# Performance work log

Measured on AMD Instinct MI355X. Metric: run time of the kernel, lower is better.

The kernel has to match this reference:

```python
import jax, jax.numpy as jnp
import numpy as np

ISIZE = 512; NHEAD = 8; NNOD = 8; MAXP = 5; NEDGE = 34; TAU = 1.0; EPS = 1e-6
B = 4; SLEN = 1024

def _ln(x, g, b):
    m = x.mean(-1, keepdims=True)
    v = ((x - m) ** 2).mean(-1, keepdims=True)
    return (x - m) * jax.lax.rsqrt(v + EPS) * g + b

def _qmask(nsrc):
    # q_mask_full: edge 0 (encoder source) is masked out for the q path
    m = np.zeros((nsrc, 5), bool); m[0, :] = True
    return m.reshape(-1)

def _routing(node_p, edge_p):
    # Host-side argmax routing; mirrors the .item() syncs in the torch forward.
    node_p = np.asarray(node_p); edge_p = np.asarray(edge_p)
    routes, lind = [], 0
    for c in range(NNOD):
        nsrc = min(c + 2, MAXP); snode = c - nsrc
        ep = edge_p[:, lind:lind + nsrc, :].reshape(3, -1)
        qm = _qmask(nsrc)
        nact = int(np.argmax(node_p[c]))
        qsel = int(np.argmax(np.where(qm, -np.inf, ep[0])))
        r = dict(lind=lind, nsrc=nsrc, snode=snode, act=nact, q=qsel, k=None, v=None, ktype=None, km=None, vmode=None)
        if nact < 7:
            km = qm if nact > 0 else None
            kl = ep[1] if km is None else np.where(km, -np.inf, ep[1])
            r['k'] = int(np.argmax(kl)); r['km'] = km
            r['ktype'] = -2 if r['k'] // 5 == 0 else -1
            if nact < 5:
                if nact == 0 and r['ktype'] == -2:
                    r['v'] = int(np.argmax(ep[2][:5])); r['vmode'] = 'first5'
                else:
                    vl = ep[2] if km is None else np.where(km, -np.inf, ep[2])
                    r['v'] = int(np.argmax(vl)); r['vmode'] = 'full'
        routes.append(r); lind += nsrc
    return routes

def _selw(logits, mask, sel):
    # GumbleNormDrop (eval): softmax over masked logits, weight of selected entry
    if mask is not None:
        logits = jnp.where(jnp.asarray(mask), -jnp.inf, logits)
    return jax.nn.softmax(logits / TAU)[sel]

def _edge_op(x, e, op, eW, eb, eg, ebe):
    # ops 0/1/2: LN->Linear with relu/gelu/identity (cost isize^2+3*isize); 3: Linear; 4: identity
    if op == 4:
        return x
    if op == 3:
        return x @ eW[e] + eb[e]
    h = _ln(x, eg[e], ebe[e]) @ eW[e] + eb[e]
    return jax.nn.relu(h) if op == 0 else (jax.nn.gelu(h) if op == 1 else h)

def _mha(q, k, v, Wn, bn, gn, bln, mask):
    Bq, Sq, D = q.shape; dh = D // NHEAD; Sk = k.shape[1]
    qn = _ln(q, gn, bln)
    qh = (qn @ Wn[0] + bn[0]).reshape(Bq, Sq, NHEAD, dh).transpose(0, 2, 1, 3)
    kh = (k @ Wn[1] + bn[1]).reshape(Bq, Sk, NHEAD, dh).transpose(0, 2, 1, 3)
    vh = (v @ Wn[2] + bn[2]).reshape(Bq, v.shape[1], NHEAD, dh).transpose(0, 2, 1, 3)
    s = jnp.einsum('bhqd,bhkd->bhqk', qh, kh) / np.float32(np.sqrt(dh))
    if mask is not None:
        s = jnp.where(mask[:, :, None, :], -1e9, s)  # [B,1,Sk] -> [B,1,1,Sk]
    o = jnp.einsum('bhqk,bhkd->bhqd', jax.nn.softmax(s, -1), vh)
    o = o.transpose(0, 2, 1, 3).reshape(Bq, Sq, D)
    return q + o @ Wn[3] + bn[3]

def _node_op(q, k, v, act, Wn, bn, gn, bln, mask):
    if act == 0: return _mha(q, k, v, Wn, bn, gn, bln, mask)
    if act == 1: return q + (jax.nn.gelu(q @ Wn[0] + bn[0]) * (k @ Wn[1] + bn[1])) @ Wn[3] + bn[3]
    if act == 2: return _ln(q + k + v, gn, bln)
    if act == 3: return q + jax.nn.relu(q @ Wn[0] + k @ Wn[1] + v @ Wn[2]) @ Wn[3] + bn[3]
    if act == 4: return q * jax.nn.sigmoid(k) + v
    if act == 5: return q + jax.nn.gelu(k @ Wn[1] + bn[1])
    if act == 6: return q + k
    return _ln(q, gn, bln)  # act 7: unary

def _forward(inpute, inputo, node_p, edge_p, eW, eb, eg, ebe, nW, nb, ng, nbe, og, obe, src_pad_mask, tgt_pad_mask, routes):
    outs = {-2: inpute, -1: inputo}
    processed = set()
    for c, r in enumerate(routes):
        lind, snode = r['lind'], r['snode']
        epq, epk, epv = (edge_p[i, lind:lind + r['nsrc'], :].reshape(-1) for i in range(3))
        qm = _qmask(r['nsrc'])
        aw = jax.nn.softmax(node_p[c] / TAU)[r['act']]
        def take(sel, logits, mask):
            se, op = sel // 5, sel % 5
            inn = -2 if se == 0 else snode + se
            processed.add(inn)
            return _selw(logits, mask, sel) * _edge_op(outs[inn], lind + se, op, eW, eb, eg, ebe)
        qv = take(r['q'], epq, qm)
        kv = take(r['k'], epk, r['km']) if r['k'] is not None else None
        if r['v'] is None:
            vv = None
        elif r['vmode'] == 'first5':
            vv = take(r['v'], epv[:5], None)
        else:
            vv = take(r['v'], epv, r['km'])
        mask = None if r['act'] == 7 else (tgt_pad_mask if r['ktype'] == -1 else src_pad_mask)
        outs[c] = aw * _node_op(qv, kv, vv, r['act'], nW[c], nb[c], ng[c], nbe[c], mask)
    rem = [outs[i] for i in range(NNOD) if i not in processed]
    o = rem[0]
    for t in rem[1:]:
        o = o + t
    return _ln(o, og, obe)

def setup_inputs():
    key = jax.random.key(0)
    ks = jax.random.split(key, 8)
    s = 0.02
    return {
        'inpute': jax.random.normal(ks[0], (B, SLEN, ISIZE), jnp.float32),
        'inputo': jax.random.normal(ks[1], (B, SLEN, ISIZE), jnp.float32),
        'node_p': jax.random.normal(ks[2], (NNOD, 8), jnp.float32),
        'edge_p': jax.random.normal(ks[3], (3, NEDGE, 5), jnp.float32),
        'edge_W': jax.random.normal(ks[4], (NEDGE, ISIZE, ISIZE), jnp.float32) * s,
        'edge_b': jnp.zeros((NEDGE, ISIZE), jnp.float32),
        'edge_g': jnp.ones((NEDGE, ISIZE), jnp.float32),
        'edge_beta': jnp.zeros((NEDGE, ISIZE), jnp.float32),
        'node_W': jax.random.normal(ks[5], (NNOD, 4, ISIZE, ISIZE), jnp.float32) * s,
        'node_b': jnp.zeros((NNOD, 4, ISIZE), jnp.float32),
        'node_g': jnp.ones((NNOD, ISIZE), jnp.float32),
        'node_beta': jnp.zeros((NNOD, ISIZE), jnp.float32),
        'out_g': jnp.ones((ISIZE,), jnp.float32),
        'out_beta': jnp.zeros((ISIZE,), jnp.float32),
        'src_pad_mask': jnp.zeros((B, 1, SLEN), bool),
        'tgt_pad_mask': jnp.zeros((B, 1, SLEN), bool),
    }

def reference(inpute, inputo, node_p, edge_p, edge_W, edge_b, edge_g, edge_beta, node_W, node_b, node_g, node_beta, out_g, out_beta, src_pad_mask, tgt_pad_mask):
    routes = _routing(node_p, edge_p)
    return _forward(inpute, inputo, node_p, edge_p, edge_W, edge_b, edge_g, edge_beta, node_W, node_b, node_g, node_beta, out_g, out_beta, src_pad_mask, tgt_pad_mask, routes)
```

## Files before the change

kernel.cpp:

```cpp
#include <hip/hip_runtime.h>
#include <hip/hip_bf16.h>
#include <math.h>

#define NTOK 4096
#define DIM  512
#define NNODC 8
#define NEDGEC 34

typedef unsigned short u16;
typedef unsigned int   u32;

typedef __attribute__((ext_vector_type(8))) short bf16x8;
typedef __attribute__((ext_vector_type(4))) float f32x4;

__device__ __forceinline__ float b2f(u16 u){ return __uint_as_float(((u32)u) << 16); }
__device__ __forceinline__ u16 f2b(float f){
    u32 x = __float_as_uint(f);
    u32 r = x + 0x7FFFu + ((x >> 16) & 1u);
    return (u16)(r >> 16);
}
__device__ __forceinline__ float ldp(const void* p, int i, int isbf){
    return isbf ? b2f(((const u16*)p)[i]) : ((const float*)p)[i];
}
__device__ __forceinline__ float gelu_t(float x){
    float x3 = x*x*x;
    return 0.5f*x*(1.0f + tanhf(0.7978845608028654f*(x + 0.044715f*x3)));
}
__device__ __forceinline__ float sigm(float x){ return 1.0f/(1.0f + expf(-x)); }

typedef __attribute__((address_space(3))) void lds_vp;
typedef __attribute__((address_space(1))) const void gbl_vp;
__device__ __forceinline__ void gload16(const u16* g, u16* l){
    __builtin_amdgcn_global_load_lds((gbl_vp*)g, (lds_vp*)l, 16, 0, 0);
}

struct Routes {
    int isbf;
    int act[NNODC];
    int q_slot[NNODC], q_e[NNODC], q_op[NNODC];
    int k_has[NNODC], k_slot[NNODC], k_e[NNODC], k_op[NNODC];
    int v_has[NNODC], v_slot[NNODC], v_e[NNODC], v_op[NNODC];
    float aw[NNODC], qw[NNODC], kw[NNODC], vw[NNODC];
    int used[NNODC];
};

__global__ void routing_kernel(const void* __restrict__ node_p,
                               const void* __restrict__ edge_p,
                               const u32* __restrict__ edge_g_probe,
                               Routes* R){
    __shared__ float ep[3*NEDGEC*5 + 2];
    __shared__ float np[NNODC*8];
    __shared__ int used_s[NNODC];
    const int tid = threadIdx.x;
    const int isbf = (edge_g_probe[0] == 0x3F803F80u) ? 1 : 0;
    for (int i = tid; i < 3*NEDGEC*5; i += 64) ep[i] = ldp(edge_p, i, isbf);
    if (tid < NNODC*8) np[tid] = ldp(node_p, tid, isbf);
    if (tid < NNODC) used_s[tid] = 0;
    __syncthreads();

    if (tid < NNODC){
        const int c = tid;
        int lind = 0;
        for (int i = 0; i < c; i++) lind += (i + 2 < 5) ? (i + 2) : 5;
        const int nsrc  = (c + 2 < 5) ? (c + 2) : 5;
        const int snode = c - nsrc;
        const int n     = nsrc * 5;

        float bm = -INFINITY; int nact = 0;
        for (int j = 0; j < 8; j++){
            float v = np[c*8 + j];
            if (v > bm){ bm = v; nact = j; }
        }
        float ssum = 0.f;
        for (int j = 0; j < 8; j++) ssum += __expf(np[c*8 + j] - bm);
        R->act[c] = nact;
        R->aw[c]  = __expf(np[c*8 + nact] - bm) / ssum;

        auto sel = [&](int phase, int nn, int maskFirst5, int* selOut, float* wOut){
            float best = -INFINITY; int bi = 0;
            for (int s2 = 0; s2 < nn; s2++){
                if (maskFirst5 && s2 < 5) continue;
                float v = ep[phase*NEDGEC*5 + (lind + s2/5)*5 + (s2%5)];
                if (v > best){ best = v; bi = s2; }
            }
            float ss = 0.f;
            for (int s2 = 0; s2 < nn; s2++){
                if (maskFirst5 && s2 < 5) continue;
                ss += __expf(ep[phase*NEDGEC*5 + (lind + s2/5)*5 + (s2%5)] - best);
            }
            *selOut = bi; *wOut = 1.0f / ss;
        };

        int qsel; float qw_;
        sel(0, n, 1, &qsel, &qw_);
        int se = qsel / 5;
        int inn = (se == 0) ? -2 : (snode + se);
        R->q_op[c] = qsel % 5; R->q_e[c] = lind + se; R->q_slot[c] = inn + 2;
        R->qw[c] = qw_;
        if (inn >= 0) used_s[inn] = 1;
        if (nact < 7){
            const int mk = (nact > 0) ? 1 : 0;
            int ksel; float kw_;
            sel(1, n, mk, &ksel, &kw_);
            se = ksel / 5; inn = (se == 0) ? -2 : (snode + se);
            R->k_has[c] = 1; R->k_op[c] = ksel % 5; R->k_e[c] = lind + se;
            R->k_slot[c] = inn + 2; R->kw[c] = kw_;
            if (inn >= 0) used_s[inn] = 1;
            if (nact < 5){
                int vsel; float vw_;
                if (nact == 0 && ksel < 5) sel(2, 5, 0, &vsel, &vw_);
                else                        sel(2, n, mk, &vsel, &vw_);
                se = vsel / 5; inn = (se == 0) ? -2 : (snode + se);
                R->v_has[c] = 1; R->v_op[c] = vsel % 5; R->v_e[c] = lind + se;
                R->v_slot[c] = inn + 2; R->vw[c] = vw_;
                if (inn >= 0) used_s[inn] = 1;
            } else { R->v_has[c] = 0; R->vw[c] = 0.f; }
        } else { R->k_has[c] = 0; R->v_has[c] = 0; R->kw[c] = 0.f; R->vw[c] = 0.f; }
    }
    __syncthreads();
    if (tid < NNODC) R->used[tid] = used_s[tid];
    if (tid == 0) R->isbf = isbf;
}

__global__ __launch_bounds__(256) void transpose_w(const void* __restrict__ eW,
                                                   const void* __restrict__ nW,
                                                   const u32* __restrict__ probe,
                                                   u16* __restrict__ Wt){
    __shared__ float tile[32][33];
    const int isbf = (probe[0] == 0x3F803F80u) ? 1 : 0;
    const int mat = blockIdx.z;
    const void* src = (mat < NEDGEC) ? eW : nW;
    const size_t moff = (size_t)((mat < NEDGEC) ? mat : (mat - NEDGEC)) * DIM * DIM;
    const int k0 = blockIdx.x*32, n0 = blockIdx.y*32;
    const int tx = threadIdx.x & 31, ty = threadIdx.x >> 5;
    #pragma unroll
    for (int r = 0; r < 32; r += 8){
        const size_t off = moff + (size_t)(k0 + r + ty)*DIM + n0 + tx;
        tile[r + ty][tx] = isbf ? b2f(((const u16*)src)[off]) : ((const float*)src)[off];
    }
    __syncthreads();
    #pragma unroll
    for (int r = 0; r < 32; r += 8){
        const size_t off = (size_t)mat*DIM*DIM + (size_t)(n0 + r + ty)*DIM + k0 + tx;
        Wt[off] = f2b(tile[tx][r + ty]);
    }
}

__global__ __launch_bounds__(256) void convert_in(const Routes* __restrict__ R,
                                                  const void* __restrict__ ie,
                                                  const void* __restrict__ io,
                                                  u16* __restrict__ Xb0,
                                                  u16* __restrict__ Xb1){
    const size_t base = ((size_t)blockIdx.x*256 + threadIdx.x) * 8;
    if (R->isbf){
        *(uint4*)(Xb0 + base) = *(const uint4*)((const u16*)ie + base);
        *(uint4*)(Xb1 + base) = *(const uint4*)((const u16*)io + base);
    } else {
        const float* a = (const float*)ie + base;
        const float* b = (const float*)io + base;
        u16 oa[8], ob[8];
        #pragma unroll
        for (int j = 0; j < 8; j++){ oa[j] = f2b(a[j]); ob[j] = f2b(b[j]); }
        *(uint4*)(Xb0 + base) = *(const uint4*)oa;
        *(uint4*)(Xb1 + base) = *(const uint4*)ob;
    }
}

struct __align__(16) LGS { u16 A[2][64*64]; u16 B[2][64*64]; };

__device__ void lean_gemm(LGS& sm, int isbf, int nsrc, int m0, int n0,
        const u16* __restrict__ A0, const u16* __restrict__ A1, const u16* __restrict__ A2,
        const u16* __restrict__ W0, const u16* __restrict__ W1, const u16* __restrict__ W2,
        const void* bias, int actMode,
        const u16* __restrict__ residB, float scale,
        u16* __restrict__ outB)
{
    const int tid = threadIdx.x;
    const int w = tid >> 6, lane = tid & 63;
    const int wr = w >> 1, wc = w & 1;
    const int l15 = lane & 15, quad = lane >> 4;
    const int NT = nsrc * 8;

    const int rsw = lane >> 3;
    const int c16 = lane & 7;
    const int rA  = w*16 + rsw;
    const size_t kcol = (size_t)((c16 ^ rsw) << 3);

    auto stage = [&](int buf, int it){
        const int s = it >> 3, kt = it & 7;
        const u16* Ab = (s == 0) ? A0 : ((s == 1) ? A1 : A2);
        const u16* Wb = (s == 0) ? W0 : ((s == 1) ? W1 : W2);
        const size_t ka = (size_t)kt*64 + kcol;
        const u16* ga = Ab + (size_t)(m0 + rA)*DIM + ka;
        const u16* gb = Wb + (size_t)(n0 + rA)*DIM + ka;
        u16* la = &sm.A[buf][rA*64 + c16*8];
        u16* lb = &sm.B[buf][rA*64 + c16*8];
        gload16(ga,          la);
        gload16(ga + 8*DIM,  la + 8*64);
        gload16(gb,          lb);
        gload16(gb + 8*DIM,  lb + 8*64);
    };

    f32x4 acc[2][2];
    #pragma unroll
    for (int i = 0; i < 2; i++)
        #pragma unroll
        for (int j = 0; j < 2; j++) acc[i][j] = (f32x4){0.f,0.f,0.f,0.f};

    stage(0, 0);
    __syncthreads();

    for (int it = 0; it < NT; it++){
        const int buf = it & 1;
        if (it + 1 < NT) stage(buf ^ 1, it + 1);
        #pragma unroll
        for (int kc = 0; kc < 2; kc++){
            const int sl = (((kc*4 + quad) ^ (l15 & 7)) << 3);
            bf16x8 af0 = *(const bf16x8*)&sm.A[buf][(wr*32      + l15)*64 + sl];
            bf16x8 af1 = *(const bf16x8*)&sm.A[buf][(wr*32 + 16 + l15)*64 + sl];
            bf16x8 bf0 = *(const bf16x8*)&sm.B[buf][(wc*32      + l15)*64 + sl];
            bf16x8 bf1 = *(const bf16x8*)&sm.B[buf][(wc*32 + 16 + l15)*64 + sl];
            acc[0][0] = __builtin_amdgcn_mfma_f32_16x16x32_bf16(af0, bf0, acc[0][0], 0, 0, 0);
            acc[0][1] = __builtin_amdgcn_mfma_f32_16x16x32_bf16(af0, bf1, acc[0][1], 0, 0, 0);
            acc[1][0] = __builtin_amdgcn_mfma_f32_16x16x32_bf16(af1, bf0, acc[1][0], 0, 0, 0);
            acc[1][1] = __builtin_amdgcn_mfma_f32_16x16x32_bf16(af1, bf1, acc[1][1], 0, 0, 0);
        }
        __syncthreads();
    }

    float* st = (float*)&sm;
    #pragma unroll
    for (int i = 0; i < 2; i++){
        #pragma unroll
        for (int j = 0; j < 2; j++){
            const int rowl = wr*32 + i*16 + quad*4;
            const int coll = wc*32 + j*16 + l15;
            const float bv = bias ? ldp(bias, n0 + coll, isbf) : 0.f;
            #pragma unroll
            for (int rg = 0; rg < 4; rg++){
                float v = acc[i][j][rg] + bv;
                if (actMode == 1) v = fmaxf(v, 0.f);
                else if (actMode == 2) v = gelu_t(v);
                st[(rowl + rg)*68 + coll] = v;
            }
        }
    }
    __syncthreads();
    #pragma unroll
    for (int t = 0; t < 2; t++){
        const int cid = tid + 256*t;
        const int rowl = cid >> 3, cg = (cid & 7)*8;
        float v[8];
        *(float4*)&v[0] = *(const float4*)&st[rowl*68 + cg];
        *(float4*)&v[4] = *(const float4*)&st[rowl*68 + cg + 4];
        const size_t go = (size_t)(m0 + rowl)*DIM + n0 + cg;
        if (residB){
            uint4 ru = *(const uint4*)(residB + go);
            const u16* rp = (const u16*)&ru;
            #pragma unroll
            for (int j2 = 0; j2 < 8; j2++) v[j2] += b2f(rp[j2]);
        }
        u16 o[8];
        #pragma unroll
        for (int j2 = 0; j2 < 8; j2++) o[j2] = f2b(v[j2]*scale);
        *(uint4*)(outB + go) = *(const uint4*)o;
    }
}

__device__ __forceinline__ void tile_remap(int* m0, int* n0){
    const int lin = blockIdx.y*64 + blockIdx.x;
    const int xcd = lin & 7, idx = lin >> 3;
    *m0 = (xcd*8 + (idx & 7)) * 64;
    *n0 = (idx >> 3) * 64;
}

__device__ __forceinline__ const void* subp(const void* p, size_t elemOff, int isbf){
    return isbf ? (const void*)((const u16*)p + elemOff) : (const void*)((const float*)p + elemOff);
}

__global__ __launch_bounds__(256) void edge_prep(const Routes* __restrict__ R, int c,
        const u16* __restrict__ Xb, u16* __restrict__ P,
        const void* eg, const void* ebeta){
    const int z = blockIdx.z;
    int has, op, e, slot;
    if (z == 0){ has = 1;            op = R->q_op[c]; e = R->q_e[c]; slot = R->q_slot[c]; }
    else if (z == 1){ has = R->k_has[c]; op = R->k_op[c]; e = R->k_e[c]; slot = R->k_slot[c]; }
    else        { has = R->v_has[c]; op = R->v_op[c]; e = R->v_e[c]; slot = R->v_slot[c]; }
    if (!has || op >= 3) return;
    const int isbf = R->isbf;
    const int tid = threadIdx.x, wid = tid >> 6, lane = tid & 63;
    const int row = blockIdx.x*4 + wid;
    const u16* src = Xb + (size_t)slot*NTOK*DIM + (size_t)row*DIM;
    u16* dst = P + (size_t)z*NTOK*DIM + (size_t)row*DIM;
    float x[8];
    #pragma unroll
    for (int j = 0; j < 2; j++){
        ushort4 u = *(const ushort4*)(src + lane*4 + j*256);
        x[j*4+0] = b2f(u.x); x[j*4+1] = b2f(u.y); x[j*4+2] = b2f(u.z); x[j*4+3] = b2f(u.w);
    }
    float s = 0.f, q = 0.f;
    #pragma unroll
    for (int j = 0; j < 8; j++){ s += x[j]; q += x[j]*x[j]; }
    #pragma unroll
    for (int m = 1; m < 64; m <<= 1){ s += __shfl_xor(s, m); q += __shfl_xor(q, m); }
    const float mu = s*(1.0f/512.0f);
    const float rstd = rsqrtf(q*(1.0f/512.0f) - mu*mu + 1e-6f);
    #pragma unroll
    for (int j = 0; j < 2; j++){
        const int col = lane*4 + j*256;
        u16 o[4];
        #pragma unroll
        for (int t = 0; t < 4; t++)
            o[t] = f2b((x[j*4+t] - mu)*rstd*ldp(eg, e*DIM + col + t, isbf) + ldp(ebeta, e*DIM + col + t, isbf));
        *(ushort4*)(dst + col) = *(const ushort4*)o;
    }
}

__global__ __launch_bounds__(256, 4) void edge_gemm(const Routes* __restrict__ R, int c,
        const u16* __restrict__ Xb, const u16* __restrict__ P,
        u16* QVb, u16* KVb, u16* VVb,
        const u16* __restrict__ Wt, const void* eb){
    __shared__ LGS sm;
    const int isbf = R->isbf;
    const int z = blockIdx.z;
    int has, slot, e, op; float w; u16* outB;
    if (z == 0){ has = 1;            slot = R->q_slot[c]; e = R->q_e[c]; op = R->q_op[c]; w = R->qw[c]; outB = QVb; }
    else if (z == 1){ has = R->k_has[c]; slot = R->k_slot[c]; e = R->k_e[c]; op = R->k_op[c]; w = R->kw[c]; outB = KVb; }
    else        { has = R->v_has[c]; slot = R->v_slot[c]; e = R->v_e[c]; op = R->v_op[c]; w = R->vw[c]; outB = VVb; }
    if (!has) return;
    if (op == 4){
        const int tid = threadIdx.x;
        const int r = blockIdx.x*64 + (tid >> 2);
        const int c0 = blockIdx.y*64 + (tid & 3)*16;
        const u16* src = Xb + (size_t)slot*NTOK*DIM + (size_t)r*DIM + c0;
        const size_t off = (size_t)r*DIM + c0;
        #pragma unroll
        for (int t = 0; t < 2; t++){
            uint4 u = *(const uint4*)(src + t*8);
            const u16* up = (const u16*)&u;
            u16 o[8];
            #pragma unroll
            for (int j = 0; j < 8; j++) o[j] = f2b(w*b2f(up[j]));
            *(uint4*)(outB + off + t*8) = *(const uint4*)o;
        }
        return;
    }
    const u16* A = (op < 3) ? (P + (size_t)z*NTOK*DIM) : (Xb + (size_t)slot*NTOK*DIM);
    const int actMode = (op == 0) ? 1 : ((op == 1) ? 2 : 0);
    int m0, n0; tile_remap(&m0, &n0);
    lean_gemm(sm, isbf, 1, m0, n0, A, nullptr, nullptr,
              Wt + (size_t)e*DIM*DIM, nullptr, nullptr,
              subp(eb, (size_t)e*DIM, isbf), actMode,
              nullptr, w, outB);
}

__global__ __launch_bounds__(256) void mid1(const Routes* __restrict__ R, int c,
        const u16* __restrict__ QVb, const u16* __restrict__ KVb, const u16* __restrict__ VVb,
        u16* __restrict__ P1, u16* __restrict__ outcb,
        const void* ng, const void* nbeta){
    const int act = R->act[c];
    if (act == 1 || act == 3 || act == 5) return;
    const int isbf = R->isbf;
    const float aw = R->aw[c];
    const int tid = threadIdx.x, wid = tid >> 6, lane = tid & 63;
    const int row = blockIdx.x*4 + wid;
    const size_t roff = (size_t)row*DIM;
    float x[8];
    #pragma unroll
    for (int j = 0; j < 2; j++){
        ushort4 u = *(const ushort4*)(QVb + roff + lane*4 + j*256);
        x[j*4+0] = b2f(u.x); x[j*4+1] = b2f(u.y); x[j*4+2] = b2f(u.z); x[j*4+3] = b2f(u.w);
    }
    if (act == 4 || act == 6 || act == 2){
        float k[8], v[8];
        #pragma unroll
        for (int j = 0; j < 2; j++){
            ushort4 u = *(const ushort4*)(KVb + roff + lane*4 + j*256);
            k[j*4+0] = b2f(u.x); k[j*4+1] = b2f(u.y); k[j*4+2] = b2f(u.z); k[j*4+3] = b2f(u.w);
        }
        if (act != 6){
            #pragma unroll
            for (int j = 0; j < 2; j++){
                ushort4 u = *(const ushort4*)(VVb + roff + lane*4 + j*256);
                v[j*4+0] = b2f(u.x); v[j*4+1] = b2f(u.y); v[j*4+2] = b2f(u.z); v[j*4+3] = b2f(u.w);
            }
        }
        if (act == 4){
            #pragma unroll
            for (int j = 0; j < 2; j++){
                u16 o[4];
                #pragma unroll
                for (int t = 0; t < 4; t++) o[t] = f2b(aw*(x[j*4+t]*sigm(k[j*4+t]) + v[j*4+t]));
                *(ushort4*)(outcb + roff + lane*4 + j*256) = *(const ushort4*)o;
            }
            return;
        }
        if (act == 6){
            #pragma unroll
            for (int j = 0; j < 2; j++){
                u16 o[4];
                #pragma unroll
                for (int t = 0; t < 4; t++) o[t] = f2b(aw*(x[j*4+t] + k[j*4+t]));
                *(ushort4*)(outcb + roff + lane*4 + j*256) = *(const ushort4*)o;
            }
            return;
        }
        #pragma unroll
        for (int j = 0; j < 8; j++) x[j] += k[j] + v[j];
    }
    float s = 0.f, q2 = 0.f;
    #pragma unroll
    for (int j = 0; j < 8; j++){ s += x[j]; q2 += x[j]*x[j]; }
    #pragma unroll
    for (int m = 1; m < 64; m <<= 1){ s += __shfl_xor(s, m); q2 += __shfl_xor(q2, m); }
    const float mu = s*(1.0f/512.0f);
    const float rstd = rsqrtf(q2*(1.0f/512.0f) - mu*mu + 1e-6f);
    const float sc = (act == 0) ? 1.0f : aw;
    u16* dst = (act == 0) ? P1 : outcb;
    #pragma unroll
    for (int j = 0; j < 2; j++){
        const int col = lane*4 + j*256;
        u16 o[4];
        #pragma unroll
        for (int t = 0; t < 4; t++)
            o[t] = f2b(sc*((x[j*4+t] - mu)*rstd*ldp(ng, c*DIM + col + t, isbf) + ldp(nbeta, c*DIM + col + t, isbf)));
        *(ushort4*)(dst + roff + col) = *(const ushort4*)o;
    }
}

__global__ __launch_bounds__(256, 4) void node_gemm_a(const Routes* __restrict__ R, int c,
        const u16* __restrict__ P1, const u16* __restrict__ QVb,
        const u16* __restrict__ KVb, const u16* __restrict__ VVb,
        u16* T1b, u16* T2b, u16* T3b,
        const u16* __restrict__ Wt, const void* nb){
    __shared__ LGS sm;
    const int isbf = R->isbf;
    const int act = R->act[c];
    const int z = blockIdx.z;
    const size_t msz = (size_t)DIM*DIM;
    const u16* W0 = Wt + (NEDGEC + (size_t)c*4 + 0)*msz;
    const u16* W1 = Wt + (NEDGEC + (size_t)c*4 + 1)*msz;
    const u16* W2 = Wt + (NEDGEC + (size_t)c*4 + 2)*msz;
    const void* b0 = subp(nb, (size_t)(c*4 + 0)*DIM, isbf);
    const void* b1 = subp(nb, (size_t)(c*4 + 1)*DIM, isbf);
    const void* b2 = subp(nb, (size_t)(c*4 + 2)*DIM, isbf);
    int m0, n0; tile_remap(&m0, &n0);
    if (z == 0){
        if (act == 0)
            lean_gemm(sm, isbf, 1, m0, n0, P1,0,0, W0,0,0, b0, 0, nullptr, 1.f, T1b);
        else if (act == 1)
            lean_gemm(sm, isbf, 1, m0, n0, QVb,0,0, W0,0,0, b0, 2, nullptr, 1.f, T1b);
        else if (act == 3)
            lean_gemm(sm, isbf, 3, m0, n0, QVb,KVb,VVb, W0,W1,W2, nullptr, 1, nullptr, 1.f, T1b);
    } else if (z == 1){
        if (act == 0 || act == 1)
            lean_gemm(sm, isbf, 1, m0, n0, KVb,0,0, W1,0,0, b1, 0, nullptr, 1.f, T2b);
        else if (act == 5)
            lean_gemm(sm, isbf, 1, m0, n0, KVb,0,0, W1,0,0, b1, 2, nullptr, 1.f, T2b);
    } else {
        if (act == 0)
            lean_gemm(sm, isbf, 1, m0, n0, VVb,0,0, W2,0,0, b2, 0, nullptr, 1.f, T3b);
    }
}

struct __align__(16) FS {
    float Qs[64][68];
    float KPs[64][68];
    float Vs[64][68];
    float red[64*16];
    float mrun[64], lrun[64], alph[64];
};

__global__ __launch_bounds__(256) void mid2(const Routes* __restrict__ R, int c,
        const u16* __restrict__ Q, const u16* __restrict__ K,
        const u16* __restrict__ V, u16* __restrict__ T4b, u16* __restrict__ P4b){
    const int act = R->act[c];
    if (act == 1){
        const int bid = blockIdx.y*32 + blockIdx.x;
        const size_t base = ((size_t)bid*256 + threadIdx.x)*16;
        #pragma unroll
        for (int h = 0; h < 2; h++){
            uint4 ua = *(const uint4*)(Q + base + h*8);
            uint4 ub = *(const uint4*)(K + base + h*8);
            const u16* pa = (const u16*)&ua;
            const u16* pb = (const u16*)&ub;
            u16 o[8];
            #pragma unroll
            for (int j = 0; j < 8; j++) o[j] = f2b(b2f(pa[j]) * b2f(pb[j]));
            *(uint4*)(P4b + base + h*8) = *(const uint4*)o;
        }
        return;
    }
    if (act != 0) return;
    __shared__ FS sm;
    const int tid = threadIdx.x;
    const int tx = tid & 15, ty = tid >> 4;
    const int b = blockIdx.x >> 3, h = blockIdx.x & 7;
    const int q0 = blockIdx.y * 64;
    const size_t baseQ = ((size_t)b*1024 + q0)*DIM + h*64;
    {
        const int r = tid >> 2, ch = tid & 3;
        const u16* qp = Q + baseQ + (size_t)r*DIM + ch*16;
        #pragma unroll
        for (int t = 0; t < 4; t++){
            ushort4 u = *(const ushort4*)(qp + t*4);
            sm.Qs[r][ch*16 + t*4 + 0] = b2f(u.x);
            sm.Qs[r][ch*16 + t*4 + 1] = b2f(u.y);
            sm.Qs[r][ch*16 + t*4 + 2] = b2f(u.z);
            sm.Qs[r][ch*16 + t*4 + 3] = b2f(u.w);
        }
    }
    if (tid < 64){ sm.mrun[tid] = -INFINITY; sm.lrun[tid] = 0.f; }
    float o[4][4];
    #pragma unroll
    for (int i = 0; i < 4; i++)
        #pragma unroll
        for (int j = 0; j < 4; j++) o[i][j] = 0.f;
    __syncthreads();

    for (int kt = 0; kt < 16; kt++){
        const size_t baseK = ((size_t)b*1024 + kt*64)*DIM + h*64;
        {
            const int r = tid >> 2, ch = tid & 3;
            const u16* kp = K + baseK + (size_t)r*DIM + ch*16;
            const u16* vp = V + baseK + (size_t)r*DIM + ch*16;
            #pragma unroll
            for (int t = 0; t < 4; t++){
                ushort4 uk = *(const ushort4*)(kp + t*4);
                ushort4 uv = *(const ushort4*)(vp + t*4);
                sm.KPs[r][ch*16 + t*4 + 0] = b2f(uk.x);
                sm.KPs[r][ch*16 + t*4 + 1] = b2f(uk.y);
                sm.KPs[r][ch*16 + t*4 + 2] = b2f(uk.z);
                sm.KPs[r][ch*16 + t*4 + 3] = b2f(uk.w);
                sm.Vs [r][ch*16 + t*4 + 0] = b2f(uv.x);
                sm.Vs [r][ch*16 + t*4 + 1] = b2f(uv.y);
                sm.Vs [r][ch*16 + t*4 + 2] = b2f(uv.z);
                sm.Vs [r][ch*16 + t*4 + 3] = b2f(uv.w);
            }
        }
        __syncthreads();
        float s[4][4];
        #pragma unroll
        for (int i = 0; i < 4; i++)
            #pragma unroll
            for (int j = 0; j < 4; j++) s[i][j] = 0.f;
        for (int d = 0; d < 64; d += 4){
            float4 qv[4], kv[4];
            #pragma unroll
            for (int i = 0; i < 4; i++) qv[i] = *(const float4*)&sm.Qs[ty*4+i][d];
            #pragma unroll
            for (int j = 0; j < 4; j++) kv[j] = *(const float4*)&sm.KPs[tx*4+j][d];
            #pragma unroll
            for (int i = 0; i < 4; i++)
                #pragma unroll
                for (int j = 0; j < 4; j++)
                    s[i][j] += qv[i].x*kv[j].x + qv[i].y*kv[j].y + qv[i].z*kv[j].z + qv[i].w*kv[j].w;
        }
        #pragma unroll
        for (int i = 0; i < 4; i++)
            #pragma unroll
            for (int j = 0; j < 4; j++) s[i][j] *= 0.125f;
        #pragma unroll
        for (int i = 0; i < 4; i++){
            float mx = fmaxf(fmaxf(s[i][0], s[i][1]), fmaxf(s[i][2], s[i][3]));
            sm.red[(ty*4+i)*16 + tx] = mx;
        }
        __syncthreads();
        if (tid < 64){
            float mt = -INFINITY;
            for (int t = 0; t < 16; t++) mt = fmaxf(mt, sm.red[tid*16+t]);
            float mold = sm.mrun[tid];
            float mnew = fmaxf(mold, mt);
            sm.alph[tid] = expf(mold - mnew);
            sm.mrun[tid] = mnew;
        }
        __syncthreads();
        #pragma unroll
        for (int i = 0; i < 4; i++){
            const float mn = sm.mrun[ty*4+i];
            float ps = 0.f;
            #pragma unroll
            for (int j = 0; j < 4; j++){
                float p = expf(s[i][j] - mn);
                sm.KPs[ty*4+i][tx*4+j] = p;
                ps += p;
            }
            sm.red[(ty*4+i)*16 + tx] = ps;
        }
        __syncthreads();
        if (tid < 64){
            float ss = 0.f;
            for (int t = 0; t < 16; t++) ss += sm.red[tid*16+t];
            sm.lrun[tid] = sm.lrun[tid]*sm.alph[tid] + ss;
        }
        __syncthreads();
        #pragma unroll
        for (int i = 0; i < 4; i++){
            const float a = sm.alph[ty*4+i];
            #pragma unroll
            for (int j = 0; j < 4; j++) o[i][j] *= a;
        }
        for (int k = 0; k < 64; k++){
            float4 v4 = *(const float4*)&sm.Vs[k][tx*4];
            float p0 = sm.KPs[ty*4+0][k];
            float p1 = sm.KPs[ty*4+1][k];
            float p2 = sm.KPs[ty*4+2][k];
            float p3 = sm.KPs[ty*4+3][k];
            o[0][0] += p0*v4.x; o[0][1] += p0*v4.y; o[0][2] += p0*v4.z; o[0][3] += p0*v4.w;
            o[1][0] += p1*v4.x; o[1][1] += p1*v4.y; o[1][2] += p1*v4.z; o[1][3] += p1*v4.w;
            o[2][0] += p2*v4.x; o[2][1] += p2*v4.y; o[2][2] += p2*v4.z; o[2][3] += p2*v4.w;
            o[3][0] += p3*v4.x; o[3][1] += p3*v4.y; o[3][2] += p3*v4.z; o[3][3] += p3*v4.w;
        }
        __syncthreads();
    }
    #pragma unroll
    for (int i = 0; i < 4; i++){
        const float inv = 1.0f / sm.lrun[ty*4+i];
        u16 ov[4];
        #pragma unroll
        for (int j = 0; j < 4; j++) ov[j] = f2b(o[i][j]*inv);
        *(ushort4*)(T4b + baseQ + (size_t)(ty*4+i)*DIM + tx*4) = *(const ushort4*)ov;
    }
}

__global__ __launch_bounds__(256, 4) void node_gemm_b(const Routes* __restrict__ R, int c,
        const u16* __restrict__ QVb, const u16* __restrict__ T1b, const u16* __restrict__ P4b,
        const u16* __restrict__ T4b, const u16* __restrict__ T2b,
        u16* outcb, const u16* __restrict__ Wt, const void* nb){
    const int act = R->act[c];
    const float aw = R->aw[c];
    if (act == 5){
        const int tid = threadIdx.x;
        const int r = blockIdx.x*64 + (tid >> 2);
        const int c0 = blockIdx.y*64 + (tid & 3)*16;
        const size_t off = (size_t)r*DIM + c0;
        #pragma unroll
        for (int t = 0; t < 2; t++){
            uint4 uq = *(const uint4*)(QVb + off + t*8);
            uint4 ug = *(const uint4*)(T2b + off + t*8);
            const u16* pq = (const u16*)&uq;
            const u16* pg = (const u16*)&ug;
            u16 o[8];
            #pragma unroll
            for (int j = 0; j < 8; j++) o[j] = f2b(aw*(b2f(pq[j]) + b2f(pg[j])));
            *(uint4*)(outcb + off + t*8) = *(const uint4*)o;
        }
        return;
    }
    if (!(act == 0 || act == 1 || act == 3)) return;
    __shared__ LGS sm;
    const int isbf = R->isbf;
    const u16* W3 = Wt + (NEDGEC + (size_t)c*4 + 3)*(size_t)DIM*DIM;
    const void* b3 = subp(nb, (size_t)(c*4 + 3)*DIM, isbf);
    const u16* A = (act == 0) ? T4b : ((act == 1) ? P4b : T1b);
    int m0, n0; tile_remap(&m0, &n0);
    lean_gemm(sm, isbf, 1, m0, n0, A, nullptr, nullptr, W3, nullptr, nullptr,
              b3, 0, QVb, aw, outcb);
}

__global__ __launch_bounds__(128) void final_ln(const Routes* __restrict__ R,
        const u16* __restrict__ Xb, const void* og, const void* obeta,
        void* __restrict__ out){
    const int isbf = R->isbf;
    const int row = blockIdx.x, tid = threadIdx.x;
    const size_t off = (size_t)row*DIM + tid*4;
    float x0 = 0.f, x1 = 0.f, x2 = 0.f, x3 = 0.f;
    for (int cc = 0; cc < NNODC; cc++){
        if (R->used[cc]) continue;
        ushort4 u = *(const ushort4*)(Xb + (size_t)(2 + cc)*NTOK*DIM + off);
        x0 += b2f(u.x); x1 += b2f(u.y); x2 += b2f(u.z); x3 += b2f(u.w);
    }
    __shared__ float rs_[128], rq_[128];
    rs_[tid] = x0 + x1 + x2 + x3;
    rq_[tid] = x0*x0 + x1*x1 + x2*x2 + x3*x3;
    __syncthreads();
    for (int st = 64; st > 0; st >>= 1){
        if (tid < st){ rs_[tid] += rs_[tid+st]; rq_[tid] += rq_[tid+st]; }
        __syncthreads();
    }
    float m = rs_[0]*(1.0f/512.0f);
    float var = rq_[0]*(1.0f/512.0f) - m*m;
    float rstd = rsqrtf(var + 1e-6f);
    float o0 = (x0 - m)*rstd*ldp(og, tid*4+0, isbf) + ldp(obeta, tid*4+0, isbf);
    float o1 = (x1 - m)*rstd*ldp(og, tid*4+1, isbf) + ldp(obeta, tid*4+1, isbf);
    float o2 = (x2 - m)*rstd*ldp(og, tid*4+2, isbf) + ldp(obeta, tid*4+2, isbf);
    float o3 = (x3 - m)*rstd*ldp(og, tid*4+3, isbf) + ldp(obeta, tid*4+3, isbf);
    if (isbf){
        u16 o[4] = { f2b(o0), f2b(o1), f2b(o2), f2b(o3) };
        *(ushort4*)((u16*)out + off) = *(const ushort4*)o;
    } else {
        float4 o; o.x = o0; o.y = o1; o.z = o2; o.w = o3;
        *(float4*)((float*)out + off) = o;
    }
}

extern "C" void kernel_launch(void* const* d_in, const int* in_sizes, int n_in,
                              void* d_out, int out_size, void* d_ws, size_t ws_size,
                              hipStream_t stream){
    (void)in_sizes; (void)n_in; (void)out_size; (void)ws_size;
    const void* inpute = d_in[0];
    const void* inputo = d_in[1];
    const void* node_p = d_in[2];
    const void* edge_p = d_in[3];
    const void* eW     = d_in[4];
    const void* eb     = d_in[5];
    const void* eg     = d_in[6];
    const void* ebeta  = d_in[7];
    const void* nW     = d_in[8];
    const void* nb     = d_in[9];
    const void* ng     = d_in[10];
    const void* nbeta  = d_in[11];
    const void* og     = d_in[12];
    const void* obeta  = d_in[13];

    const size_t SZ = (size_t)NTOK * DIM;
    char* ws = (char*)d_ws;
    u16* Wt = (u16*)ws;
    char* p = ws + (size_t)66*DIM*DIM*2;
    Routes* R = (Routes*)p; p += 1024;
    u16* Xb  = (u16*)p;  p += 10*SZ*2;
    u16* QVb = (u16*)p; p += SZ*2;
    u16* KVb = (u16*)p; p += SZ*2;
    u16* VVb = (u16*)p; p += SZ*2;
    u16* P   = (u16*)p; p += 3*SZ*2;
    u16* T1b = (u16*)p; p += SZ*2;
    u16* T2b = (u16*)p; p += SZ*2;
    u16* T3b = (u16*)p; p += SZ*2;
    u16* T4b = (u16*)p; p += SZ*2;
    u16* P4b = (u16*)p; p += SZ*2;

    routing_kernel<<<1, 64, 0, stream>>>(node_p, edge_p, (const u32*)eg, R);
    transpose_w<<<dim3(16, 16, 66), 256, 0, stream>>>(eW, nW, (const u32*)eg, Wt);
    convert_in<<<1024, 256, 0, stream>>>(R, inpute, inputo, Xb, Xb + SZ);

    for (int c = 0; c < NNODC; c++){
        u16* outcb = Xb + (size_t)(2 + c)*SZ;
        edge_prep  <<<dim3(1024, 1, 3), 256, 0, stream>>>(R, c, Xb, P, eg, ebeta);
        edge_gemm  <<<dim3(64, 8, 3), 256, 0, stream>>>(R, c, Xb, P, QVb, KVb, VVb, Wt, eb);
        mid1       <<<1024, 256, 0, stream>>>(R, c, QVb, KVb, VVb, P , outcb, ng, nbeta);
        node_gemm_a<<<dim3(64, 8, 3), 256, 0, stream>>>(R, c, P , QVb, KVb, VVb, T1b, T2b, T3b, Wt, nb);
        mid2       <<<dim3(32, 16), 256, 0, stream>>>(R, c, T1b, T2b, T3b, T4b, P4b);
        node_gemm_b<<<dim3(64, 8), 256, 0, stream>>>(R, c, QVb, T1b, P4b, T4b, T2b, outcb, Wt, nb);
    }
    final_ln<<<4096, 128, 0, stream>>>(R, Xb, og, obeta, d_out);
}
```

Before: 555.1 us.

## Enlarge GEMM tiles to 128x128 and skip transposing unused weight matrices

The shared GEMM routine moves from 64x64 to 128x128 output tiles, with each wave computing a 4x4 grid of MFMA accumulators. Launch grids, tile remapping, the identity/elementwise paths and launch bounds are updated to match. The aim is more data reuse per LDS load and fewer blocks, at the cost of more registers, lower occupancy and fewer blocks to fill the CUs (at most 128 per GEMM launch). Separately, the routing kernel now records which edge and node weight matrices are actually used, and the transpose kernel skips the rest to cut weight-conversion traffic.

```diff
diff --git a/kernel.cpp b/kernel.cpp
--- a/kernel.cpp
+++ b/kernel.cpp
@@ -42,6 +42,7 @@
     int v_has[NNODC], v_slot[NNODC], v_e[NNODC], v_op[NNODC];
     float aw[NNODC], qw[NNODC], kw[NNODC], vw[NNODC];
     int used[NNODC];
+    int need[66];
 };
 
 __global__ void routing_kernel(const void* __restrict__ node_p,
@@ -51,11 +52,13 @@
     __shared__ float ep[3*NEDGEC*5 + 2];
     __shared__ float np[NNODC*8];
     __shared__ int used_s[NNODC];
+    __shared__ int need_s[66];
     const int tid = threadIdx.x;
     const int isbf = (edge_g_probe[0] == 0x3F803F80u) ? 1 : 0;
     for (int i = tid; i < 3*NEDGEC*5; i += 64) ep[i] = ldp(edge_p, i, isbf);
     if (tid < NNODC*8) np[tid] = ldp(node_p, tid, isbf);
     if (tid < NNODC) used_s[tid] = 0;
+    for (int i = tid; i < 66; i += 64) need_s[i] = 0;
     __syncthreads();
 
     if (tid < NNODC){
@@ -75,6 +78,11 @@
         for (int j = 0; j < 8; j++) ssum += __expf(np[c*8 + j] - bm);
         R->act[c] = nact;
         R->aw[c]  = __expf(np[c*8 + nact] - bm) / ssum;
+
+        const int nb0 = NEDGEC + c*4;
+        if (nact == 0 || nact == 3){ need_s[nb0]=1; need_s[nb0+1]=1; need_s[nb0+2]=1; need_s[nb0+3]=1; }
+        else if (nact == 1){ need_s[nb0]=1; need_s[nb0+1]=1; need_s[nb0+3]=1; }
+        else if (nact == 5){ need_s[nb0+1]=1; }
 
         auto sel = [&](int phase, int nn, int maskFirst5, int* selOut, float* wOut){
             float best = -INFINITY; int bi = 0;
@@ -97,6 +105,7 @@
         int inn = (se == 0) ? -2 : (snode + se);
         R->q_op[c] = qsel % 5; R->q_e[c] = lind + se; R->q_slot[c] = inn + 2;
         R->qw[c] = qw_;
+        if (qsel % 5 != 4) need_s[lind + se] = 1;
         if (inn >= 0) used_s[inn] = 1;
         if (nact < 7){
             const int mk = (nact > 0) ? 1 : 0;
@@ -105,6 +114,7 @@
             se = ksel / 5; inn = (se == 0) ? -2 : (snode + se);
             R->k_has[c] = 1; R->k_op[c] = ksel % 5; R->k_e[c] = lind + se;
             R->k_slot[c] = inn + 2; R->kw[c] = kw_;
+            if (ksel % 5 != 4) need_s[lind + se] = 1;
             if (inn >= 0) used_s[inn] = 1;
             if (nact < 5){
                 int vsel; float vw_;
@@ -113,22 +123,26 @@
                 se = vsel / 5; inn = (se == 0) ? -2 : (snode + se);
                 R->v_has[c] = 1; R->v_op[c] = vsel % 5; R->v_e[c] = lind + se;
                 R->v_slot[c] = inn + 2; R->vw[c] = vw_;
+                if (vsel % 5 != 4) need_s[lind + se] = 1;
                 if (inn >= 0) used_s[inn] = 1;
             } else { R->v_has[c] = 0; R->vw[c] = 0.f; }
         } else { R->k_has[c] = 0; R->v_has[c] = 0; R->kw[c] = 0.f; R->vw[c] = 0.f; }
     }
     __syncthreads();
     if (tid < NNODC) R->used[tid] = used_s[tid];
+    for (int i = tid; i < 66; i += 64) R->need[i] = need_s[i];
     if (tid == 0) R->isbf = isbf;
 }
 
-__global__ __launch_bounds__(256) void transpose_w(const void* __restrict__ eW,
+__global__ __launch_bounds__(256) void transpose_w(const Routes* __restrict__ R,
+                                                   const void* __restrict__ eW,
                                                    const void* __restrict__ nW,
                                                    const u32* __restrict__ probe,
                                                    u16* __restrict__ Wt){
     __shared__ float tile[32][33];
+    const int mat = blockIdx.z;
+    if (!R->need[mat]) return;
     const int isbf = (probe[0] == 0x3F803F80u) ? 1 : 0;
-    const int mat = blockIdx.z;
     const void* src = (mat < NEDGEC) ? eW : nW;
     const size_t moff = (size_t)((mat < NEDGEC) ? mat : (mat - NEDGEC)) * DIM * DIM;
     const int k0 = blockIdx.x*32, n0 = blockIdx.y*32;
@@ -166,15 +180,17 @@
     }
 }
 
-struct __align__(16) LGS { u16 A[2][64*64]; u16 B[2][64*64]; };
-
-__device__ void lean_gemm(LGS& sm, int isbf, int nsrc, int m0, int n0,
+struct __align__(16) LGS { u16 A[2][128*64]; u16 B[2][128*64]; };
+union  __align__(16) LGU { LGS g; float st[128*132]; };
+
+__device__ void lean_gemm(LGU& smu, int isbf, int nsrc, int m0, int n0,
         const u16* __restrict__ A0, const u16* __restrict__ A1, const u16* __restrict__ A2,
         const u16* __restrict__ W0, const u16* __restrict__ W1, const u16* __restrict__ W2,
         const void* bias, int actMode,
         const u16* __restrict__ residB, float scale,
         u16* __restrict__ outB)
 {
+    LGS& sm = smu.g;
     const int tid = threadIdx.x;
     const int w = tid >> 6, lane = tid & 63;
     const int wr = w >> 1, wc = w & 1;
@@ -183,29 +199,27 @@
 
     const int rsw = lane >> 3;
     const int c16 = lane & 7;
-    const int rA  = w*16 + rsw;
-    const size_t kcol = (size_t)((c16 ^ rsw) << 3);
+    const int rA  = w*8 + rsw;
+    const int kx  = (c16 ^ rsw) << 3;
 
     auto stage = [&](int buf, int it){
         const int s = it >> 3, kt = it & 7;
         const u16* Ab = (s == 0) ? A0 : ((s == 1) ? A1 : A2);
         const u16* Wb = (s == 0) ? W0 : ((s == 1) ? W1 : W2);
-        const size_t ka = (size_t)kt*64 + kcol;
-        const u16* ga = Ab + (size_t)(m0 + rA)*DIM + ka;
-        const u16* gb = Wb + (size_t)(n0 + rA)*DIM + ka;
-        u16* la = &sm.A[buf][rA*64 + c16*8];
-        u16* lb = &sm.B[buf][rA*64 + c16*8];
-        gload16(ga,          la);
-        gload16(ga + 8*DIM,  la + 8*64);
-        gload16(gb,          lb);
-        gload16(gb + 8*DIM,  lb + 8*64);
+        const size_t ka = (size_t)kt*64 + kx;
+        #pragma unroll
+        for (int i = 0; i < 4; i++){
+            const int r = rA + i*32;
+            gload16(Ab + (size_t)(m0 + r)*DIM + ka, &sm.A[buf][r*64 + c16*8]);
+            gload16(Wb + (size_t)(n0 + r)*DIM + ka, &sm.B[buf][r*64 + c16*8]);
+        }
     };
 
-    f32x4 acc[2][2];
-    #pragma unroll
-    for (int i = 0; i < 2; i++)
-        #pragma unroll
-        for (int j = 0; j < 2; j++) acc[i][j] = (f32x4){0.f,0.f,0.f,0.f};
+    f32x4 acc[4][4];
+    #pragma unroll
+    for (int i = 0; i < 4; i++)
+        #pragma unroll
+        for (int j = 0; j < 4; j++) acc[i][j] = (f32x4){0.f,0.f,0.f,0.f};
 
     stage(0, 0);
     __syncthreads();
@@ -215,44 +229,48 @@
         if (it + 1 < NT) stage(buf ^ 1, it + 1);
         #pragma unroll
         for (int kc = 0; kc < 2; kc++){
-            const int sl = (((kc*4 + quad) ^ (l15 & 7)) << 3);
-            bf16x8 af0 = *(const bf16x8*)&sm.A[buf][(wr*32      + l15)*64 + sl];
-            bf16x8 af1 = *(const bf16x8*)&sm.A[buf][(wr*32 + 16 + l15)*64 + sl];
-            bf16x8 bf0 = *(const bf16x8*)&sm.B[buf][(wc*32      + l15)*64 + sl];
-            bf16x8 bf1 = *(const bf16x8*)&sm.B[buf][(wc*32 + 16 + l15)*64 + sl];
-            acc[0][0] = __builtin_amdgcn_mfma_f32_16x16x32_bf16(af0, bf0, acc[0][0], 0, 0, 0);
-            acc[0][1] = __builtin_amdgcn_mfma_f32_16x16x32_bf16(af0, bf1, acc[0][1], 0, 0, 0);
-            acc[1][0] = __builtin_amdgcn_mfma_f32_16x16x32_bf16(af1, bf0, acc[1][0], 0, 0, 0);
-            acc[1][1] = __builtin_amdgcn_mfma_f32_16x16x32_bf16(af1, bf1, acc[1][1], 0, 0, 0);
+            const int sl = ((kc*4 + quad) ^ (l15 & 7)) << 3;
+            bf16x8 af[4], bv[4];
+            #pragma unroll
+            for (int i = 0; i < 4; i++)
+                af[i] = *(const bf16x8*)&sm.A[buf][(wr*64 + i*16 + l15)*64 + sl];
+            #pragma unroll
+            for (int j = 0; j < 4; j++)
+                bv[j] = *(const bf16x8*)&sm.B[buf][(wc*64 + j*16 + l15)*64 + sl];
+            #pragma unroll
+            for (int i = 0; i < 4; i++)
+                #pragma unroll
+                for (int j = 0; j < 4; j++)
+                    acc[i][j] = __builtin_amdgcn_mfma_f32_16x16x32_bf16(af[i], bv[j], acc[i][j], 0, 0, 0);
         }
         __syncthreads();
     }
 
-    float* st = (float*)&sm;
-    #pragma unroll
-    for (int i = 0; i < 2; i++){
-        #pragma unroll
-        for (int j = 0; j < 2; j++){
-            const int rowl = wr*32 + i*16 + quad*4;
-            const int coll = wc*32 + j*16 + l15;
-            const float bv = bias ? ldp(bias, n0 + coll, isbf) : 0.f;
+    float* st = smu.st;
+    #pragma unroll
+    for (int i = 0; i < 4; i++){
+        #pragma unroll
+        for (int j = 0; j < 4; j++){
+            const int rowl = wr*64 + i*16 + quad*4;
+            const int coll = wc*64 + j*16 + l15;
+            const float bvs = bias ? ldp(bias, n0 + coll, isbf) : 0.f;
             #pragma unroll
             for (int rg = 0; rg < 4; rg++){
-                float v = acc[i][j][rg] + bv;
+                float v = acc[i][j][rg] + bvs;
                 if (actMode == 1) v = fmaxf(v, 0.f);
                 else if (actMode == 2) v = gelu_t(v);
-                st[(rowl + rg)*68 + coll] = v;
+                st[(rowl + rg)*132 + coll] = v;
             }
         }
     }
     __syncthreads();
     #pragma unroll
-    for (int t = 0; t < 2; t++){
+    for (int t = 0; t < 8; t++){
         const int cid = tid + 256*t;
-        const int rowl = cid >> 3, cg = (cid & 7)*8;
+        const int rowl = cid >> 4, cg = (cid & 15)*8;
         float v[8];
-        *(float4*)&v[0] = *(const float4*)&st[rowl*68 + cg];
-        *(float4*)&v[4] = *(const float4*)&st[rowl*68 + cg + 4];
+        *(float4*)&v[0] = *(const float4*)&st[rowl*132 + cg];
+        *(float4*)&v[4] = *(const float4*)&st[rowl*132 + cg + 4];
         const size_t go = (size_t)(m0 + rowl)*DIM + n0 + cg;
         if (residB){
             uint4 ru = *(const uint4*)(residB + go);
@@ -268,10 +286,10 @@
 }
 
 __device__ __forceinline__ void tile_remap(int* m0, int* n0){
-    const int lin = blockIdx.y*64 + blockIdx.x;
+    const int lin = blockIdx.y*32 + blockIdx.x;
     const int xcd = lin & 7, idx = lin >> 3;
-    *m0 = (xcd*8 + (idx & 7)) * 64;
-    *n0 = (idx >> 3) * 64;
+    *m0 = (xcd*4 + (idx & 3)) * 128;
+    *n0 = (idx >> 2) * 128;
 }
 
 __device__ __forceinline__ const void* subp(const void* p, size_t elemOff, int isbf){
@@ -316,11 +334,11 @@
     }
 }
 
-__global__ __launch_bounds__(256, 4) void edge_gemm(const Routes* __restrict__ R, int c,
+__global__ __launch_bounds__(256, 2) void edge_gemm(const Routes* __restrict__ R, int c,
         const u16* __restrict__ Xb, const u16* __restrict__ P,
         u16* QVb, u16* KVb, u16* VVb,
         const u16* __restrict__ Wt, const void* eb){
-    __shared__ LGS sm;
+    __shared__ LGU sm;
     const int isbf = R->isbf;
     const int z = blockIdx.z;
     int has, slot, e, op; float w; u16* outB;
@@ -330,18 +348,18 @@
     if (!has) return;
     if (op == 4){
         const int tid = threadIdx.x;
-        const int r = blockIdx.x*64 + (tid >> 2);
-        const int c0 = blockIdx.y*64 + (tid & 3)*16;
+        const int r  = blockIdx.x*128 + (tid >> 1);
+        const int c0 = blockIdx.y*128 + (tid & 1)*64;
         const u16* src = Xb + (size_t)slot*NTOK*DIM + (size_t)r*DIM + c0;
-        const size_t off = (size_t)r*DIM + c0;
-        #pragma unroll
-        for (int t = 0; t < 2; t++){
+        u16* dst = outB + (size_t)r*DIM + c0;
+        #pragma unroll
+        for (int t = 0; t < 8; t++){
             uint4 u = *(const uint4*)(src + t*8);
             const u16* up = (const u16*)&u;
             u16 o[8];
             #pragma unroll
             for (int j = 0; j < 8; j++) o[j] = f2b(w*b2f(up[j]));
-            *(uint4*)(outB + off + t*8) = *(const uint4*)o;
+            *(uint4*)(dst + t*8) = *(const uint4*)o;
         }
         return;
     }
@@ -428,12 +446,12 @@
     }
 }
 
-__global__ __launch_bounds__(256, 4) void node_gemm_a(const Routes* __restrict__ R, int c,
+__global__ __launch_bounds__(256, 2) void node_gemm_a(const Routes* __restrict__ R, int c,
         const u16* __restrict__ P1, const u16* __restrict__ QVb,
         const u16* __restrict__ KVb, const u16* __restrict__ VVb,
         u16* T1b, u16* T2b, u16* T3b,
         const u16* __restrict__ Wt, const void* nb){
-    __shared__ LGS sm;
+    __shared__ LGU sm;
     const int isbf = R->isbf;
     const int act = R->act[c];
     const int z = blockIdx.z;
@@ -623,7 +641,7 @@
     }
 }
 
-__global__ __launch_bounds__(256, 4) void node_gemm_b(const Routes* __restrict__ R, int c,
+__global__ __launch_bounds__(256, 2) void node_gemm_b(const Routes* __restrict__ R, int c,
         const u16* __restrict__ QVb, const u16* __restrict__ T1b, const u16* __restrict__ P4b,
         const u16* __restrict__ T4b, const u16* __restrict__ T2b,
         u16* outcb, const u16* __restrict__ Wt, const void* nb){
@@ -631,11 +649,11 @@
     const float aw = R->aw[c];
     if (act == 5){
         const int tid = threadIdx.x;
-        const int r = blockIdx.x*64 + (tid >> 2);
-        const int c0 = blockIdx.y*64 + (tid & 3)*16;
+        const int r  = blockIdx.x*128 + (tid >> 1);
+        const int c0 = blockIdx.y*128 + (tid & 1)*64;
         const size_t off = (size_t)r*DIM + c0;
         #pragma unroll
-        for (int t = 0; t < 2; t++){
+        for (int t = 0; t < 8; t++){
             uint4 uq = *(const uint4*)(QVb + off + t*8);
             uint4 ug = *(const uint4*)(T2b + off + t*8);
             const u16* pq = (const u16*)&uq;
@@ -648,7 +666,7 @@
         return;
     }
     if (!(act == 0 || act == 1 || act == 3)) return;
-    __shared__ LGS sm;
+    __shared__ LGU sm;
     const int isbf = R->isbf;
     const u16* W3 = Wt + (NEDGEC + (size_t)c*4 + 3)*(size_t)DIM*DIM;
     const void* b3 = subp(nb, (size_t)(c*4 + 3)*DIM, isbf);
@@ -730,17 +748,17 @@
     u16* P4b = (u16*)p; p += SZ*2;
 
     routing_kernel<<<1, 64, 0, stream>>>(node_p, edge_p, (const u32*)eg, R);
-    transpose_w<<<dim3(16, 16, 66), 256, 0, stream>>>(eW, nW, (const u32*)eg, Wt);
+    transpose_w<<<dim3(16, 16, 66), 256, 0, stream>>>(R, eW, nW, (const u32*)eg, Wt);
     convert_in<<<1024, 256, 0, stream>>>(R, inpute, inputo, Xb, Xb + SZ);
 
     for (int c = 0; c < NNODC; c++){
         u16* outcb = Xb + (size_t)(2 + c)*SZ;
         edge_prep  <<<dim3(1024, 1, 3), 256, 0, stream>>>(R, c, Xb, P, eg, ebeta);
-        edge_gemm  <<<dim3(64, 8, 3), 256, 0, stream>>>(R, c, Xb, P, QVb, KVb, VVb, Wt, eb);
+        edge_gemm  <<<dim3(32, 4, 3), 256, 0, stream>>>(R, c, Xb, P, QVb, KVb, VVb, Wt, eb);
         mid1       <<<1024, 256, 0, stream>>>(R, c, QVb, KVb, VVb, P , outcb, ng, nbeta);
-        node_gemm_a<<<dim3(64, 8, 3), 256, 0, stream>>>(R, c, P , QVb, KVb, VVb, T1b, T2b, T3b, Wt, nb);
+        node_gemm_a<<<dim3(32, 4, 3), 256, 0, stream>>>(R, c, P , QVb, KVb, VVb, T1b, T2b, T3b, Wt, nb);
         mid2       <<<dim3(32, 16), 256, 0, stream>>>(R, c, T1b, T2b, T3b, T4b, P4b);
-        node_gemm_b<<<dim3(64, 8), 256, 0, stream>>>(R, c, QVb, T1b, P4b, T4b, T2b, outcb, Wt, nb);
+        node_gemm_b<<<dim3(32, 4), 256, 0, stream>>>(R, c, QVb, T1b, P4b, T4b, T2b, outcb, Wt, nb);
     }
     final_ln<<<4096, 128, 0, stream>>>(R, Xb, og, obeta, d_out);
 }
```

Result: slower. 741.9 us (+33.6%).
